# Kernel tuning notes

Measured on AMD Instinct MI355X. Metric: run time of the kernel, lower is better.

The kernel has to match this reference:

```python
import jax, jax.numpy as jnp
import numpy as np

VOCAB = 32000
EMB = 512       # embedding_size; also the sequence length per the source loop
HID = 512       # hidden_dim
NTAG = 36       # number of POS-tag-specific LSTMCells
OUT = 1         # output_size
SEQ = EMB       # forward iterates range(embedding_size)


def setup_inputs() -> dict:
    key = jax.random.key(0)
    ks = jax.random.split(key, 10)
    s = 1.0 / np.sqrt(HID)  # torch LSTMCell init: U(-1/sqrt(H), 1/sqrt(H))
    inp = {
        "x": jax.random.randint(ks[0], (1, SEQ), 0, VOCAB, dtype=jnp.int64)
             if jax.config.jax_enable_x64 else
             jax.random.randint(ks[0], (1, SEQ), 0, VOCAB, dtype=jnp.int32),
        "tag_ids": jax.random.randint(ks[1], (SEQ,), 0, NTAG, dtype=jnp.int32),
        "h0": jnp.zeros((1, HID), jnp.float32),
        "c0": jnp.zeros((1, HID), jnp.float32),
        # frozen pretrained embedding table
        "emb": jax.random.normal(ks[2], (VOCAB, EMB), jnp.float32) * 0.1,
        # stacked per-tag LSTMCell params, torch gate order (i, f, g, o)
        "W_ih": jax.random.uniform(ks[3], (NTAG, 4 * HID, EMB), jnp.float32, -s, s),
        "W_hh": jax.random.uniform(ks[4], (NTAG, 4 * HID, HID), jnp.float32, -s, s),
        "b_ih": jax.random.uniform(ks[5], (NTAG, 4 * HID), jnp.float32, -s, s),
        "b_hh": jax.random.uniform(ks[6], (NTAG, 4 * HID), jnp.float32, -s, s),
        "W_fc": jax.random.uniform(ks[7], (OUT, HID), jnp.float32, -s, s),
        "b_fc": jax.random.uniform(ks[8], (OUT,), jnp.float32, -s, s),
    }
    return inp


def _lstm_cell(x_t, h, c, Wih, Whh, bih, bhh):
    # x_t: [D], h/c: [H]; Wih: [4H, D], Whh: [4H, H]
    gates = Wih @ x_t + Whh @ h + bih + bhh      # [4H]
    i, f, g, o = jnp.split(gates, 4)
    i, f, o = jax.nn.sigmoid(i), jax.nn.sigmoid(f), jax.nn.sigmoid(o)
    g = jnp.tanh(g)
    c_new = f * c + i * g
    h_new = o * jnp.tanh(c_new)
    return h_new, c_new


def reference(x, tag_ids, h0, c0, emb, W_ih, W_hh, b_ih, b_hh, W_fc, b_fc):
    embeds = emb[x[0]]                            # [T, D] (batch is structurally 1)

    def step(carry, xs):
        h, c = carry
        x_t, tag = xs
        h, c = _lstm_cell(x_t, h, c, W_ih[tag], W_hh[tag], b_ih[tag], b_hh[tag])
        return (h, c), None

    (h, c), _ = jax.lax.scan(step, (h0[0], c0[0]), (embeds, tag_ids))
    # dropout is identity in eval; fc + sigmoid; out[:, -1]
    out = jax.nn.sigmoid(h @ W_fc.T + b_fc)       # [OUT]
    out = out.reshape(1, -1)[:, -1]               # [1]
    return out, h[None, :], c[None, :]
```

## Files before the change

kernel.cpp:

```cpp
#include <hip/hip_runtime.h>

#define VOCAB 32000
#define EMB 512
#define HID 512
#define NTAG 36
#define SEQ 512
#define G4H 2048
#define NBLK 128
#define XCHUNK 32

typedef unsigned long long ull;

__global__ __launch_bounds__(256) void precompute_z(
    const int* __restrict__ x,
    const int* __restrict__ tag_ids,
    const float* __restrict__ emb,
    const float* __restrict__ W_ih,
    const float* __restrict__ b_ih,
    const float* __restrict__ b_hh,
    float* __restrict__ Z)
{
    __shared__ int list[SEQ];
    __shared__ int cnt;
    __shared__ __align__(16) float xc[XCHUNK][EMB];

    const int tid  = threadIdx.x;
    const int tag  = blockIdx.x;
    const int row0 = blockIdx.y * 64;
    const int wave = tid >> 6, lane = tid & 63;

    if (tid == 0) cnt = 0;
    __syncthreads();
    for (int t = tid; t < SEQ; t += 256)
        if (tag_ids[t] == tag) { int p = atomicAdd(&cnt, 1); list[p] = t; }
    __syncthreads();
    const int n = cnt;

    for (int c0 = 0; c0 < n; c0 += XCHUNK) {
        const int nc = min(XCHUNK, n - c0);
        __syncthreads();
        for (int idx = tid; idx < nc * EMB; idx += 256) {
            int tl = idx >> 9, k = idx & 511;
            int t = list[c0 + tl];
            xc[tl][k] = emb[(size_t)x[t] * EMB + k];
        }
        __syncthreads();
        for (int rr = 0; rr < 16; rr += 4) {
            const int row = row0 + wave * 16 + rr;
            const float* w0p = W_ih + ((size_t)tag * G4H + row) * EMB;
            const float* w1p = w0p + EMB;
            const float* w2p = w0p + 2 * EMB;
            const float* w3p = w0p + 3 * EMB;
            const float4 wa0 = ((const float4*)w0p)[lane], wa1 = ((const float4*)w0p)[64 + lane];
            const float4 wb0 = ((const float4*)w1p)[lane], wb1 = ((const float4*)w1p)[64 + lane];
            const float4 wc0 = ((const float4*)w2p)[lane], wc1 = ((const float4*)w2p)[64 + lane];
            const float4 wd0 = ((const float4*)w3p)[lane], wd1 = ((const float4*)w3p)[64 + lane];
            const float bi0 = b_ih[tag * G4H + row]     + b_hh[tag * G4H + row];
            const float bi1 = b_ih[tag * G4H + row + 1] + b_hh[tag * G4H + row + 1];
            const float bi2 = b_ih[tag * G4H + row + 2] + b_hh[tag * G4H + row + 2];
            const float bi3 = b_ih[tag * G4H + row + 3] + b_hh[tag * G4H + row + 3];
            for (int tl = 0; tl < nc; ++tl) {
                float4 x0 = *(const float4*)&xc[tl][4 * lane];
                float4 x1 = *(const float4*)&xc[tl][256 + 4 * lane];
                float d0 = wa0.x*x0.x + wa0.y*x0.y + wa0.z*x0.z + wa0.w*x0.w
                         + wa1.x*x1.x + wa1.y*x1.y + wa1.z*x1.z + wa1.w*x1.w;
                float d1 = wb0.x*x0.x + wb0.y*x0.y + wb0.z*x0.z + wb0.w*x0.w
                         + wb1.x*x1.x + wb1.y*x1.y + wb1.z*x1.z + wb1.w*x1.w;
                float d2 = wc0.x*x0.x + wc0.y*x0.y + wc0.z*x0.z + wc0.w*x0.w
                         + wc1.x*x1.x + wc1.y*x1.y + wc1.z*x1.z + wc1.w*x1.w;
                float d3 = wd0.x*x0.x + wd0.y*x0.y + wd0.z*x0.z + wd0.w*x0.w
                         + wd1.x*x1.x + wd1.y*x1.y + wd1.z*x1.z + wd1.w*x1.w;
                #pragma unroll
                for (int m = 32; m >= 1; m >>= 1) {
                    d0 += __shfl_xor(d0, m, 64);
                    d1 += __shfl_xor(d1, m, 64);
                    d2 += __shfl_xor(d2, m, 64);
                    d3 += __shfl_xor(d3, m, 64);
                }
                if (lane == 0) {
                    float* zr = Z + (size_t)list[c0 + tl] * G4H + row;
                    zr[0] = d0 + bi0; zr[1] = d1 + bi1;
                    zr[2] = d2 + bi2; zr[3] = d3 + bi3;
                }
            }
        }
    }
}

__global__ __launch_bounds__(256) void lstm_seq(
    const int* __restrict__ tag_ids,
    const float* __restrict__ h0,
    const float* __restrict__ c0,
    const float* __restrict__ W_hh,
    const float* __restrict__ Z,
    const float* __restrict__ W_fc,
    const float* __restrict__ b_fc,
    ull* __restrict__ hist,
    float* __restrict__ d_out)
{
    __shared__ int tags[SEQ];
    __shared__ __align__(16) float hsh[2][HID];
    __shared__ float red[256];

    const int tid  = threadIdx.x;
    const int b    = blockIdx.x;
    const int wave = tid >> 6, lane = tid & 63;
    const int j    = b * 4 + wave;

    for (int t = tid; t < SEQ; t += 256) tags[t] = tag_ids[t];
    __syncthreads();

    float c    = (lane == 0) ? c0[j] : 0.f;
    float hval = 0.f;

    for (int t = 0; t < SEQ; ++t) {
        const int tag = tags[t];
        const float* wbase = W_hh + (size_t)tag * G4H * HID;
        const float4* r;
        r = (const float4*)(wbase + (size_t)(j)        * HID);
        float4 wi0 = r[lane], wi1 = r[64 + lane];
        r = (const float4*)(wbase + (size_t)(512 + j)  * HID);
        float4 wf0 = r[lane], wf1 = r[64 + lane];
        r = (const float4*)(wbase + (size_t)(1024 + j) * HID);
        float4 wg0 = r[lane], wg1 = r[64 + lane];
        r = (const float4*)(wbase + (size_t)(1536 + j) * HID);
        float4 wo0 = r[lane], wo1 = r[64 + lane];

        float zi = 0.f, zf = 0.f, zg = 0.f, zo = 0.f;
        if (lane == 0) {
            const float* zt = Z + (size_t)t * G4H;
            zi = zt[j]; zf = zt[512 + j]; zg = zt[1024 + j]; zo = zt[1536 + j];
        }

        float v0, v1;
        if (t == 0) {
            v0 = h0[2 * tid]; v1 = h0[2 * tid + 1];
        } else {
            const ull* hp = hist + (size_t)(t - 1) * HID;
            ull a  = __hip_atomic_load(&hp[2 * tid],     __ATOMIC_RELAXED, __HIP_MEMORY_SCOPE_AGENT);
            ull bq = __hip_atomic_load(&hp[2 * tid + 1], __ATOMIC_RELAXED, __HIP_MEMORY_SCOPE_AGENT);
            while ((unsigned)(a >> 32) != (unsigned)t || (unsigned)(bq >> 32) != (unsigned)t) {
                __builtin_amdgcn_s_sleep(1);
                a  = __hip_atomic_load(&hp[2 * tid],     __ATOMIC_RELAXED, __HIP_MEMORY_SCOPE_AGENT);
                bq = __hip_atomic_load(&hp[2 * tid + 1], __ATOMIC_RELAXED, __HIP_MEMORY_SCOPE_AGENT);
            }
            v0 = __uint_as_float((unsigned)a);
            v1 = __uint_as_float((unsigned)bq);
        }
        const int hb = t & 1;
        hsh[hb][2 * tid]     = v0;
        hsh[hb][2 * tid + 1] = v1;
        __syncthreads();

        const float4 ha = *(const float4*)&hsh[hb][4 * lane];
        const float4 hc = *(const float4*)&hsh[hb][256 + 4 * lane];

        float di = wi0.x*ha.x + wi0.y*ha.y + wi0.z*ha.z + wi0.w*ha.w
                 + wi1.x*hc.x + wi1.y*hc.y + wi1.z*hc.z + wi1.w*hc.w;
        float df = wf0.x*ha.x + wf0.y*ha.y + wf0.z*ha.z + wf0.w*ha.w
                 + wf1.x*hc.x + wf1.y*hc.y + wf1.z*hc.z + wf1.w*hc.w;
        float dg = wg0.x*ha.x + wg0.y*ha.y + wg0.z*ha.z + wg0.w*ha.w
                 + wg1.x*hc.x + wg1.y*hc.y + wg1.z*hc.z + wg1.w*hc.w;
        float do_ = wo0.x*ha.x + wo0.y*ha.y + wo0.z*ha.z + wo0.w*ha.w
                  + wo1.x*hc.x + wo1.y*hc.y + wo1.z*hc.z + wo1.w*hc.w;
        #pragma unroll
        for (int m = 32; m >= 1; m >>= 1) {
            di  += __shfl_xor(di,  m, 64);
            df  += __shfl_xor(df,  m, 64);
            dg  += __shfl_xor(dg,  m, 64);
            do_ += __shfl_xor(do_, m, 64);
        }

        if (lane == 0) {
            float gi = zi + di, gf = zf + df, gg = zg + dg, go = zo + do_;
            float si = 1.f / (1.f + __expf(-gi));
            float sf = 1.f / (1.f + __expf(-gf));
            float so = 1.f / (1.f + __expf(-go));
            float tg = tanhf(gg);
            c = sf * c + si * tg;
            hval = so * tanhf(c);
            ull pk = ((ull)(unsigned)(t + 1) << 32) | (ull)__float_as_uint(hval);
            __hip_atomic_store(&hist[(size_t)t * HID + j], pk,
                               __ATOMIC_RELAXED, __HIP_MEMORY_SCOPE_AGENT);
        }
    }

    if (lane == 0) {
        d_out[1 + j]       = hval;
        d_out[1 + HID + j] = c;
    }

    if (b == 0) {
        const ull* hp = hist + (size_t)(SEQ - 1) * HID;
        ull a  = __hip_atomic_load(&hp[2 * tid],     __ATOMIC_RELAXED, __HIP_MEMORY_SCOPE_AGENT);
        ull bq = __hip_atomic_load(&hp[2 * tid + 1], __ATOMIC_RELAXED, __HIP_MEMORY_SCOPE_AGENT);
        while ((unsigned)(a >> 32) != (unsigned)SEQ || (unsigned)(bq >> 32) != (unsigned)SEQ) {
            __builtin_amdgcn_s_sleep(1);
            a  = __hip_atomic_load(&hp[2 * tid],     __ATOMIC_RELAXED, __HIP_MEMORY_SCOPE_AGENT);
            bq = __hip_atomic_load(&hp[2 * tid + 1], __ATOMIC_RELAXED, __HIP_MEMORY_SCOPE_AGENT);
        }
        float s = __uint_as_float((unsigned)a)  * W_fc[2 * tid]
                + __uint_as_float((unsigned)bq) * W_fc[2 * tid + 1];
        red[tid] = s;
        __syncthreads();
        #pragma unroll
        for (int off = 128; off > 0; off >>= 1) {
            if (tid < off) red[tid] += red[tid + off];
            __syncthreads();
        }
        if (tid == 0)
            d_out[0] = 1.f / (1.f + __expf(-(red[0] + b_fc[0])));
    }
}

extern "C" void kernel_launch(void* const* d_in, const int* in_sizes, int n_in,
                              void* d_out, int out_size, void* d_ws, size_t ws_size,
                              hipStream_t stream) {
    const int*   x       = (const int*)d_in[0];
    const int*   tag_ids = (const int*)d_in[1];
    const float* h0      = (const float*)d_in[2];
    const float* c0      = (const float*)d_in[3];
    const float* emb     = (const float*)d_in[4];
    const float* W_ih    = (const float*)d_in[5];
    const float* W_hh    = (const float*)d_in[6];
    const float* b_ih    = (const float*)d_in[7];
    const float* b_hh    = (const float*)d_in[8];
    const float* W_fc    = (const float*)d_in[9];
    const float* b_fc    = (const float*)d_in[10];
    float* out = (float*)d_out;

    float* Z    = (float*)d_ws;
    ull*   hist = (ull*)((char*)d_ws + (size_t)SEQ * G4H * sizeof(float));

    dim3 gA(NTAG, 32);
    precompute_z<<<gA, 256, 0, stream>>>(x, tag_ids, emb, W_ih, b_ih, b_hh, Z);
    lstm_seq<<<NBLK, 256, 0, stream>>>(tag_ids, h0, c0, W_hh, Z, W_fc, b_fc,
                                       hist, out);
}
```

Before: 1.408 ms.

## Pipeline spin-wait loads, drop sleeps, vectorize embedding gather, use fast tanh

```diff
diff --git a/kernel.cpp b/kernel.cpp
--- a/kernel.cpp
+++ b/kernel.cpp
@@ -10,6 +10,14 @@
 #define XCHUNK 32
 
 typedef unsigned long long ull;
+
+__device__ __forceinline__ float fast_tanh(float x) {
+    float e = __expf(2.f * x);
+    return 1.f - 2.f / (e + 1.f);
+}
+__device__ __forceinline__ float fast_sigmoid(float x) {
+    return 1.f / (1.f + __expf(-x));
+}
 
 __global__ __launch_bounds__(256) void precompute_z(
     const int* __restrict__ x,
@@ -39,10 +47,10 @@
     for (int c0 = 0; c0 < n; c0 += XCHUNK) {
         const int nc = min(XCHUNK, n - c0);
         __syncthreads();
-        for (int idx = tid; idx < nc * EMB; idx += 256) {
-            int tl = idx >> 9, k = idx & 511;
+        for (int idx = tid; idx < nc * 128; idx += 256) {
+            int tl = idx >> 7, k4 = idx & 127;
             int t = list[c0 + tl];
-            xc[tl][k] = emb[(size_t)x[t] * EMB + k];
+            ((float4*)xc[tl])[k4] = ((const float4*)(emb + (size_t)x[t] * EMB))[k4];
         }
         __syncthreads();
         for (int rr = 0; rr < 16; rr += 4) {
@@ -132,20 +140,29 @@
             zi = zt[j]; zf = zt[512 + j]; zg = zt[1024 + j]; zo = zt[1536 + j];
         }
 
+        asm volatile("s_waitcnt vmcnt(0)" ::: "memory");
+
         float v0, v1;
         if (t == 0) {
             v0 = h0[2 * tid]; v1 = h0[2 * tid + 1];
         } else {
-            const ull* hp = hist + (size_t)(t - 1) * HID;
-            ull a  = __hip_atomic_load(&hp[2 * tid],     __ATOMIC_RELAXED, __HIP_MEMORY_SCOPE_AGENT);
-            ull bq = __hip_atomic_load(&hp[2 * tid + 1], __ATOMIC_RELAXED, __HIP_MEMORY_SCOPE_AGENT);
-            while ((unsigned)(a >> 32) != (unsigned)t || (unsigned)(bq >> 32) != (unsigned)t) {
-                __builtin_amdgcn_s_sleep(1);
-                a  = __hip_atomic_load(&hp[2 * tid],     __ATOMIC_RELAXED, __HIP_MEMORY_SCOPE_AGENT);
-                bq = __hip_atomic_load(&hp[2 * tid + 1], __ATOMIC_RELAXED, __HIP_MEMORY_SCOPE_AGENT);
+            const ull* pa = hist + (size_t)(t - 1) * HID + 2 * tid;
+            const ull* pb = pa + 1;
+            const unsigned want = (unsigned)t;
+            ull a0 = __hip_atomic_load(pa, __ATOMIC_RELAXED, __HIP_MEMORY_SCOPE_AGENT);
+            ull b0 = __hip_atomic_load(pb, __ATOMIC_RELAXED, __HIP_MEMORY_SCOPE_AGENT);
+            ull a1 = __hip_atomic_load(pa, __ATOMIC_RELAXED, __HIP_MEMORY_SCOPE_AGENT);
+            ull b1 = __hip_atomic_load(pb, __ATOMIC_RELAXED, __HIP_MEMORY_SCOPE_AGENT);
+            ull a2 = __hip_atomic_load(pa, __ATOMIC_RELAXED, __HIP_MEMORY_SCOPE_AGENT);
+            ull b2 = __hip_atomic_load(pb, __ATOMIC_RELAXED, __HIP_MEMORY_SCOPE_AGENT);
+            while ((unsigned)(a0 >> 32) != want || (unsigned)(b0 >> 32) != want) {
+                a0 = a1; b0 = b1;
+                a1 = a2; b1 = b2;
+                a2 = __hip_atomic_load(pa, __ATOMIC_RELAXED, __HIP_MEMORY_SCOPE_AGENT);
+                b2 = __hip_atomic_load(pb, __ATOMIC_RELAXED, __HIP_MEMORY_SCOPE_AGENT);
             }
-            v0 = __uint_as_float((unsigned)a);
-            v1 = __uint_as_float((unsigned)bq);
+            v0 = __uint_as_float((unsigned)a0);
+            v1 = __uint_as_float((unsigned)b0);
         }
         const int hb = t & 1;
         hsh[hb][2 * tid]     = v0;
@@ -173,12 +190,12 @@
 
         if (lane == 0) {
             float gi = zi + di, gf = zf + df, gg = zg + dg, go = zo + do_;
-            float si = 1.f / (1.f + __expf(-gi));
-            float sf = 1.f / (1.f + __expf(-gf));
-            float so = 1.f / (1.f + __expf(-go));
-            float tg = tanhf(gg);
+            float si = fast_sigmoid(gi);
+            float sf = fast_sigmoid(gf);
+            float so = fast_sigmoid(go);
+            float tg = fast_tanh(gg);
             c = sf * c + si * tg;
-            hval = so * tanhf(c);
+            hval = so * fast_tanh(c);
             ull pk = ((ull)(unsigned)(t + 1) << 32) | (ull)__float_as_uint(hval);
             __hip_atomic_store(&hist[(size_t)t * HID + j], pk,
                                __ATOMIC_RELAXED, __HIP_MEMORY_SCOPE_AGENT);
@@ -195,7 +212,6 @@
         ull a  = __hip_atomic_load(&hp[2 * tid],     __ATOMIC_RELAXED, __HIP_MEMORY_SCOPE_AGENT);
         ull bq = __hip_atomic_load(&hp[2 * tid + 1], __ATOMIC_RELAXED, __HIP_MEMORY_SCOPE_AGENT);
         while ((unsigned)(a >> 32) != (unsigned)SEQ || (unsigned)(bq >> 32) != (unsigned)SEQ) {
-            __builtin_amdgcn_s_sleep(1);
             a  = __hip_atomic_load(&hp[2 * tid],     __ATOMIC_RELAXED, __HIP_MEMORY_SCOPE_AGENT);
             bq = __hip_atomic_load(&hp[2 * tid + 1], __ATOMIC_RELAXED, __HIP_MEMORY_SCOPE_AGENT);
         }
@@ -209,7 +225,7 @@
             __syncthreads();
         }
         if (tid == 0)
-            d_out[0] = 1.f / (1.f + __expf(-(red[0] + b_fc[0])));
+            d_out[0] = fast_sigmoid(red[0] + b_fc[0]);
     }
 }
 
@@ -229,8 +245,9 @@
     const float* b_fc    = (const float*)d_in[10];
     float* out = (float*)d_out;
 
+    const size_t zBytes = (size_t)SEQ * G4H * sizeof(float);
     float* Z    = (float*)d_ws;
-    ull*   hist = (ull*)((char*)d_ws + (size_t)SEQ * G4H * sizeof(float));
+    ull*   hist = (ull*)((char*)d_ws + zBytes);
 
     dim3 gA(NTAG, 32);
     precompute_z<<<gA, 256, 0, stream>>>(x, tag_ids, emb, W_ih, b_ih, b_hh, Z);
```

Result: faster. 1.329 ms (-5.6%).
